# Optimization experiments

Hardware: AMD Instinct MI355X
Metric: run time of the kernel (lower is better)

The kernel has to match this reference:

```python
import jax, jax.numpy as jnp
import numpy as np

D = 128            # actual_dim / embed_dim
DM = 2 * D         # d_model
HID = 2 * DM       # LSTMCell hidden size
NSYM = 200000
PAD = NSYM
B = 4096
S = 5
NB = 64
STEPS = 4
EPS = 1e-6


def setup_inputs() -> dict:
    key = jax.random.key(0)
    ks = jax.random.split(key, 24)
    def rn(k, sh, scale=0.02):
        return jax.random.normal(k, sh, dtype=jnp.float32) * scale
    emb = rn(ks[10], (NSYM + 1, D)).at[PAD].set(0.0)  # padding row zeroed
    inp = {
        'query': jax.random.randint(ks[0], (B, 2), 0, NSYM),
        'support': jax.random.randint(ks[1], (S, 2), 0, NSYM),
        'q_l_conn': jax.random.randint(ks[2], (B, NB, 2), 0, NSYM),
        'q_l_deg': jax.random.randint(ks[3], (B,), 0, NB),
        'q_r_conn': jax.random.randint(ks[4], (B, NB, 2), 0, NSYM),
        'q_r_deg': jax.random.randint(ks[5], (B,), 0, NB),
        's_l_conn': jax.random.randint(ks[6], (S, NB, 2), 0, NSYM),
        's_l_deg': jax.random.randint(ks[7], (S,), 0, NB),
        's_r_conn': jax.random.randint(ks[8], (S, NB, 2), 0, NSYM),
        's_r_deg': jax.random.randint(ks[9], (S,), 0, NB),
        'emb': emb,
        'gcn_w': rn(ks[11], (D, 2 * D)),
        'gcn_bias': jnp.zeros((D,), jnp.float32),
        'proj1_w': rn(ks[12], (2 * DM, DM)),
        'proj1_b': jnp.zeros((2 * DM,), jnp.float32),
        'proj2_w': rn(ks[13], (DM, 2 * DM)),
        'proj2_b': jnp.zeros((DM,), jnp.float32),
        'ln_g': jnp.ones((DM,), jnp.float32),
        'ln_b': jnp.zeros((DM,), jnp.float32),
        'w_ih': rn(ks[14], (4 * HID, DM)),
        'w_hh': rn(ks[15], (4 * HID, HID)),
        'b_ih': jnp.zeros((4 * HID,), jnp.float32),
        'b_hh': jnp.zeros((4 * HID,), jnp.float32),
    }
    return inp


def _neighbor_encoder(conn, deg, emb, gcn_w, gcn_bias):
    # conn: [N, NB, 2] ids (rel, ent); deg: [N]
    rel = emb[conn[:, :, 0]]                     # [N, NB, D] gather
    ent = emb[conn[:, :, 1]]                     # [N, NB, D] gather
    x = jnp.concatenate([rel, ent], axis=-1)     # [N, NB, 2D]
    out = jnp.einsum('bnd,kd->bnk', x, gcn_w) + gcn_bias  # [N, NB, D]
    denom = jnp.maximum(deg, 1).astype(out.dtype)[:, None]
    return jnp.tanh(out.sum(axis=1) / denom)     # [N, D]


def _support_encoder(x, proj1_w, proj1_b, proj2_w, proj2_b, ln_g, ln_b):
    residual = x
    h = jax.nn.relu(x @ proj1_w.T + proj1_b)
    h = h @ proj2_w.T + proj2_b
    z = h + residual
    mu = z.mean(axis=-1, keepdims=True)
    sigma = jnp.std(z, axis=-1, keepdims=True, ddof=1)
    return ln_g * (z - mu) / (sigma + EPS) + ln_b


def _query_encoder(support_vec, query, w_ih, w_hh, b_ih, b_hh):
    # support_vec: [DM] (single support prototype); query: [B, DM]
    bsz = query.shape[0]
    h_r = jnp.zeros((bsz, HID), query.dtype)
    c = jnp.zeros((bsz, HID), query.dtype)
    xW = query @ w_ih.T + b_ih  # invariant across steps
    h = query
    for _ in range(STEPS):
        gates = xW + h_r @ w_hh.T + b_hh
        i, f, g, o = jnp.split(gates, 4, axis=-1)
        c = jax.nn.sigmoid(f) * c + jax.nn.sigmoid(i) * jnp.tanh(g)
        h_cell = jax.nn.sigmoid(o) * jnp.tanh(c)
        h = query + h_cell[:, :DM]
        # attention over a single support row: softmax of one logit == 1
        r = jnp.broadcast_to(support_vec[None, :], h.shape)
        h_r = jnp.concatenate([h, r], axis=-1)
    return h


def reference(query, support, q_l_conn, q_l_deg, q_r_conn, q_r_deg,
              s_l_conn, s_l_deg, s_r_conn, s_r_deg,
              emb, gcn_w, gcn_bias, proj1_w, proj1_b, proj2_w, proj2_b,
              ln_g, ln_b, w_ih, w_hh, b_ih, b_hh):
    ql = _neighbor_encoder(q_l_conn, q_l_deg, emb, gcn_w, gcn_bias)
    qr = _neighbor_encoder(q_r_conn, q_r_deg, emb, gcn_w, gcn_bias)
    sl = _neighbor_encoder(s_l_conn, s_l_deg, emb, gcn_w, gcn_bias)
    sr = _neighbor_encoder(s_r_conn, s_r_deg, emb, gcn_w, gcn_bias)
    query_nb = jnp.concatenate([ql, qr], axis=-1)    # [B, DM]
    support_nb = jnp.concatenate([sl, sr], axis=-1)  # [S, DM]
    se = lambda x: _support_encoder(x, proj1_w, proj1_b, proj2_w, proj2_b, ln_g, ln_b)
    support_g = se(support_nb).mean(axis=0)          # [DM]
    query_g = se(query_nb)                            # [B, DM]
    query_f = _query_encoder(support_g, query_g, w_ih, w_hh, b_ih, b_hh)
    qn = query_f / jnp.maximum(jnp.linalg.norm(query_f, axis=-1, keepdims=True), 1e-12)
    sn = support_g / jnp.maximum(jnp.linalg.norm(support_g), 1e-12)
    return qn @ sn                                    # [B] matching scores
```

## Files before the change

### kernel.cpp

```cpp
#include <hip/hip_runtime.h>

#define BQ 4096
#define NS 5

typedef __attribute__((ext_vector_type(8))) short bf16x8;
typedef __attribute__((ext_vector_type(4))) float f32x4;
typedef unsigned short ushortT;

#define WS_QNB    0
#define WS_Z      1048576
#define WS_QG     2097152
#define WS_XW     3145728
#define WS_CBUF   5242880
#define WS_XS     6291456
#define WS_H1B    7348224
#define WS_ABF    7872512
#define WS_HB1    8134656
#define WS_P1B    8396800
#define WS_P2B    8462336
#define WS_WIHB   8527872
#define WS_WHHB   8658944
#define WS_GWB    8790016
#define WS_SNB    8806400
#define WS_H1G    8807680
#define WS_ZB     8810240
#define WS_SG     8811520
#define WS_SN     8811776
#define WS_SWL    8812032
#define WS_BL     8813056

__device__ __forceinline__ float wave_allreduce(float v) {
#pragma unroll
  for (int off = 32; off > 0; off >>= 1) v += __shfl_xor(v, off, 64);
  return v;
}
__device__ __forceinline__ float block_allreduce(float v, float* buf) {
  v = wave_allreduce(v);
  __syncthreads();
  if ((threadIdx.x & 63) == 0) buf[threadIdx.x >> 6] = v;
  __syncthreads();
  return buf[0] + buf[1] + buf[2] + buf[3];
}
__device__ __forceinline__ float sigm(float x) { return 1.0f / (1.0f + expf(-x)); }
__device__ __forceinline__ ushortT f2bf(float f) {
  unsigned int u = __float_as_uint(f);
  unsigned int r = (u + 0x7fffu + ((u >> 16) & 1u)) >> 16;
  return (ushortT)r;
}
__device__ __forceinline__ float bf2f(ushortT u) {
  return __uint_as_float(((unsigned int)u) << 16);
}
__device__ __forceinline__ float dot4(float4 a, float4 b) {
  return a.x * b.x + a.y * b.y + a.z * b.z + a.w * b.w;
}

__global__ void k_pack(const float* __restrict__ w_ih, const float* __restrict__ w_hh,
                       const float* __restrict__ p1w, const float* __restrict__ p2w,
                       const float* __restrict__ gcn_w,
                       const float* __restrict__ b_ih, const float* __restrict__ b_hh,
                       ushortT* __restrict__ p1b16, ushortT* __restrict__ p2b16,
                       ushortT* __restrict__ wihb, ushortT* __restrict__ whhb,
                       ushortT* __restrict__ gwb, float* __restrict__ bL) {
  const int stride = gridDim.x * blockDim.x;
  const int gid = blockIdx.x * blockDim.x + threadIdx.x;
  for (int i = gid; i < 131072; i += stride) p1b16[i] = f2bf(p1w[i]);
  for (int i = gid; i < 131072; i += stride) p2b16[i] = f2bf(p2w[i]);
  for (int i = gid; i < 262144; i += stride) {
    int n = i >> 8, k = i & 255;
    int j = (n >> 2) + 512 * (n & 3);
    wihb[i] = f2bf(w_ih[j * 256 + k]);
    whhb[i] = f2bf(w_hh[j * 512 + k]);
  }
  for (int i = gid; i < 32768; i += stride) gwb[i] = f2bf(gcn_w[i]);
  for (int i = gid; i < 1024; i += stride) {
    int j = (i >> 2) + 512 * (i & 3);
    bL[i] = b_ih[j] + b_hh[j];
  }
}

__global__ __launch_bounds__(256) void k_gather(
    const int* __restrict__ qlc, const int* __restrict__ qrc,
    const int* __restrict__ slc, const int* __restrict__ src_,
    const float* __restrict__ emb, ushortT* __restrict__ XS) {
  const int r = blockIdx.x;
  const int b = r >> 1, side = r & 1;
  const int t = threadIdx.x;
  const int* cg;
  if (b < BQ) cg = (side ? qrc : qlc) + (size_t)b * 128;
  else        cg = (side ? src_ : slc) + (size_t)(b - BQ) * 128;
  __shared__ int connS[128];
  __shared__ __align__(16) float part[8][132];
  if (t < 128) connS[t] = cg[t];
  __syncthreads();
  const int s = t >> 5, l = t & 31;
  const float4* emb4 = (const float4*)emb;
  float4 acc = make_float4(0.f, 0.f, 0.f, 0.f);
#pragma unroll
  for (int kb = 0; kb < 2; kb++) {
    int im[8];
#pragma unroll
    for (int k = 0; k < 8; k++) im[k] = connS[(kb * 8 + k) * 8 + s];
    float4 v[8];
#pragma unroll
    for (int k = 0; k < 8; k++) v[k] = emb4[(size_t)im[k] * 32 + l];
#pragma unroll
    for (int k = 0; k < 8; k++) {
      acc.x += v[k].x; acc.y += v[k].y; acc.z += v[k].z; acc.w += v[k].w;
    }
  }
  *(float4*)&part[s][l * 4] = acc;
  __syncthreads();
  const int hf = t >> 7, dd = t & 127;
  float sum = part[hf][dd] + part[2 + hf][dd] + part[4 + hf][dd] + part[6 + hf][dd];
  XS[(size_t)r * 256 + t] = f2bf(sum);
}

__global__ __launch_bounds__(256) void k_gcn(
    const ushortT* __restrict__ XS, const ushortT* __restrict__ gwb,
    const float* __restrict__ gcn_bias,
    const int* __restrict__ qld, const int* __restrict__ qrd,
    const int* __restrict__ sld, const int* __restrict__ srd,
    float* __restrict__ qnb, float* __restrict__ snb, ushortT* __restrict__ xq) {
  __shared__ short As[64 * 40];
  __shared__ short Bs[128 * 40];
  __shared__ int degl[32], degr[32];
  const int t = threadIdx.x;
  const int row0 = blockIdx.x * 64;
  if (t < 32) {
    int b = (row0 >> 1) + t;
    int dl = 1, dr = 1;
    if (b < BQ) { dl = qld[b]; dr = qrd[b]; }
    else if (b < BQ + NS) { dl = sld[b - BQ]; dr = srd[b - BQ]; }
    degl[t] = (dl > 0) ? dl : 1;
    degr[t] = (dr > 0) ? dr : 1;
  }
  const int wave = t >> 6, lane = t & 63;
  const int wm = wave >> 1, wn = wave & 1, quad = lane >> 4, mr = lane & 15;
  f32x4 acc[2][4];
#pragma unroll
  for (int mi = 0; mi < 2; mi++)
#pragma unroll
    for (int ni = 0; ni < 4; ni++) acc[mi][ni] = (f32x4){0.f, 0.f, 0.f, 0.f};
  const int arow = t >> 2, akc = t & 3;
  for (int k0 = 0; k0 < 256; k0 += 32) {
    float4 av = *(const float4*)(XS + (size_t)(row0 + arow) * 256 + k0 + akc * 8);
    float4 bv0 = *(const float4*)(gwb + (size_t)arow * 256 + k0 + akc * 8);
    float4 bv1 = *(const float4*)(gwb + (size_t)(64 + arow) * 256 + k0 + akc * 8);
    __syncthreads();
    *(float4*)&As[arow * 40 + akc * 8] = av;
    *(float4*)&Bs[arow * 40 + akc * 8] = bv0;
    *(float4*)&Bs[(64 + arow) * 40 + akc * 8] = bv1;
    __syncthreads();
    bf16x8 af[2], bfr[4];
#pragma unroll
    for (int mi = 0; mi < 2; mi++)
      af[mi] = *(const bf16x8*)&As[(wm * 32 + mi * 16 + mr) * 40 + quad * 8];
#pragma unroll
    for (int ni = 0; ni < 4; ni++)
      bfr[ni] = *(const bf16x8*)&Bs[(wn * 64 + ni * 16 + mr) * 40 + quad * 8];
#pragma unroll
    for (int mi = 0; mi < 2; mi++)
#pragma unroll
      for (int ni = 0; ni < 4; ni++)
        acc[mi][ni] = __builtin_amdgcn_mfma_f32_16x16x32_bf16(af[mi], bfr[ni], acc[mi][ni], 0, 0, 0);
  }
#pragma unroll
  for (int mi = 0; mi < 2; mi++) {
#pragma unroll
    for (int ni = 0; ni < 4; ni++) {
      const int col = wn * 64 + ni * 16 + mr;
      const int rb = row0 + wm * 32 + mi * 16 + quad * 4;
      const float bs = 64.0f * gcn_bias[col];
#pragma unroll
      for (int reg = 0; reg < 4; reg++) {
        const int row = rb + reg;
        const int b = row >> 1, side = row & 1;
        if (b >= BQ + NS) continue;
        const int li = (row >> 1) - (row0 >> 1);
        const int deg = side ? degr[li] : degl[li];
        float val = tanhf((acc[mi][ni][reg] + bs) / (float)deg);
        if (b < BQ) {
          const size_t o = (size_t)b * 256 + side * 128 + col;
          qnb[o] = val;
          xq[o] = f2bf(val);
        } else {
          snb[(size_t)(b - BQ) * 256 + side * 128 + col] = val;
        }
      }
    }
  }
}

__global__ __launch_bounds__(256) void k_sup1(
    const float* __restrict__ snb, const float* __restrict__ p1w,
    const float* __restrict__ p1b, float* __restrict__ h1g) {
  const int w = blockIdx.x * 4 + (threadIdx.x >> 6);
  const int lane = threadIdx.x & 63;
  const int r = w >> 9, j = w & 511;
  float4 x = *(const float4*)&snb[r * 256 + lane * 4];
  float4 wv = *(const float4*)&p1w[(size_t)j * 256 + lane * 4];
  float s = wave_allreduce(dot4(x, wv));
  if (lane == 0) h1g[r * 512 + j] = fmaxf(s + p1b[j], 0.f);
}

__global__ __launch_bounds__(256) void k_sup2(
    const float* __restrict__ snb, const float* __restrict__ h1g,
    const float* __restrict__ p2w, const float* __restrict__ p2b,
    float* __restrict__ zb) {
  const int w = blockIdx.x * 4 + (threadIdx.x >> 6);
  const int lane = threadIdx.x & 63;
  const int r = w >> 8, tt = w & 255;
  float4 h0 = *(const float4*)&h1g[r * 512 + lane * 4];
  float4 h1 = *(const float4*)&h1g[r * 512 + 256 + lane * 4];
  float4 w0 = *(const float4*)&p2w[(size_t)tt * 512 + lane * 4];
  float4 w1 = *(const float4*)&p2w[(size_t)tt * 512 + 256 + lane * 4];
  float s = wave_allreduce(dot4(h0, w0) + dot4(h1, w1));
  if (lane == 0) zb[r * 256 + tt] = s + p2b[tt] + snb[r * 256 + tt];
}

__global__ __launch_bounds__(256) void k_sup3(
    const float* __restrict__ zb, const float* __restrict__ ln_g,
    const float* __restrict__ ln_b, float* __restrict__ sg, float* __restrict__ sn) {
  const int t = threadIdx.x;
  __shared__ float rbuf[4];
  float acc = 0.f;
  for (int r = 0; r < NS; r++) {
    float z = zb[r * 256 + t];
    float s = block_allreduce(z, rbuf);
    float mu = s * (1.f / 256.f);
    float dz = z - mu;
    float s2 = block_allreduce(dz * dz, rbuf);
    float rstd = 1.f / (sqrtf(s2 * (1.f / 255.f)) + 1e-6f);
    acc += ln_g[t] * dz * rstd + ln_b[t];
    __syncthreads();
  }
  float g = acc * (1.f / (float)NS);
  sg[t] = g;
  float n2 = block_allreduce(g * g, rbuf);
  sn[t] = g / fmaxf(sqrtf(n2), 1e-12f);
}

__global__ __launch_bounds__(256) void k_sup4(
    const float* __restrict__ sg, const float* __restrict__ w_hh,
    float* __restrict__ sWl) {
  const int n = blockIdx.x * 4 + (threadIdx.x >> 6);
  const int lane = threadIdx.x & 63;
  const int j = (n >> 2) + 512 * (n & 3);
  float4 x = *(const float4*)&sg[lane * 4];
  float4 wv = *(const float4*)&w_hh[(size_t)j * 512 + 256 + lane * 4];
  float s = wave_allreduce(dot4(x, wv));
  if (lane == 0) sWl[n] = s;
}

__global__ __launch_bounds__(256) void k_gemm(
    const ushortT* __restrict__ A, const ushortT* __restrict__ B,
    const float* __restrict__ bias, const float* __restrict__ aux,
    float* __restrict__ outf, ushortT* __restrict__ outb,
    int K, int N, int nbn, int mode) {
  __shared__ short As[64 * 40];
  __shared__ short Bs[128 * 40];
  const int t = threadIdx.x;
  const int bn = blockIdx.x % nbn, bm = blockIdx.x / nbn;
  const int row0 = bm * 64, col0 = bn * 128;
  const int wave = t >> 6, lane = t & 63;
  const int wm = wave >> 1, wn = wave & 1, quad = lane >> 4, mr = lane & 15;
  f32x4 acc[2][4];
#pragma unroll
  for (int mi = 0; mi < 2; mi++)
#pragma unroll
    for (int ni = 0; ni < 4; ni++) acc[mi][ni] = (f32x4){0.f, 0.f, 0.f, 0.f};
  const int arow = t >> 2, akc = t & 3;
  for (int k0 = 0; k0 < K; k0 += 32) {
    float4 av = *(const float4*)(A + (size_t)(row0 + arow) * K + k0 + akc * 8);
    float4 bv0 = *(const float4*)(B + (size_t)(col0 + arow) * K + k0 + akc * 8);
    float4 bv1 = *(const float4*)(B + (size_t)(col0 + 64 + arow) * K + k0 + akc * 8);
    __syncthreads();
    *(float4*)&As[arow * 40 + akc * 8] = av;
    *(float4*)&Bs[arow * 40 + akc * 8] = bv0;
    *(float4*)&Bs[(64 + arow) * 40 + akc * 8] = bv1;
    __syncthreads();
    bf16x8 af[2], bfr[4];
#pragma unroll
    for (int mi = 0; mi < 2; mi++)
      af[mi] = *(const bf16x8*)&As[(wm * 32 + mi * 16 + mr) * 40 + quad * 8];
#pragma unroll
    for (int ni = 0; ni < 4; ni++)
      bfr[ni] = *(const bf16x8*)&Bs[(wn * 64 + ni * 16 + mr) * 40 + quad * 8];
#pragma unroll
    for (int mi = 0; mi < 2; mi++)
#pragma unroll
      for (int ni = 0; ni < 4; ni++)
        acc[mi][ni] = __builtin_amdgcn_mfma_f32_16x16x32_bf16(af[mi], bfr[ni], acc[mi][ni], 0, 0, 0);
  }
#pragma unroll
  for (int mi = 0; mi < 2; mi++) {
#pragma unroll
    for (int ni = 0; ni < 4; ni++) {
      const int col = col0 + wn * 64 + ni * 16 + mr;
      const int rb = row0 + wm * 32 + mi * 16 + quad * 4;
      const float bs = bias[col];
#pragma unroll
      for (int reg = 0; reg < 4; reg++) {
        const int row = rb + reg;
        const size_t off = (size_t)row * N + col;
        float v = acc[mi][ni][reg];
        if (mode == 0) outb[off] = f2bf(fmaxf(v + bs, 0.f));
        else outf[off] = v + bs + aux[off];
      }
    }
  }
}

__global__ __launch_bounds__(256) void k_gemm_lstm(
    const ushortT* __restrict__ A, const ushortT* __restrict__ B,
    const float* __restrict__ bL, const float* __restrict__ sWl,
    const float* __restrict__ qg, ushortT* __restrict__ xwb,
    float* __restrict__ cbuf, ushortT* __restrict__ hb_out, int phase) {
  __shared__ short As[64 * 40];
  __shared__ short Bs[128 * 40];
  __shared__ __align__(16) float Cs[64 * 132];
  const int t = threadIdx.x;
  const int bn = blockIdx.x & 7, bm = blockIdx.x >> 3;
  const int row0 = bm * 64, col0 = bn * 128;
  const int wave = t >> 6, lane = t & 63;
  const int wm = wave >> 1, wn = wave & 1, quad = lane >> 4, mr = lane & 15;
  f32x4 acc[2][4];
#pragma unroll
  for (int mi = 0; mi < 2; mi++)
#pragma unroll
    for (int ni = 0; ni < 4; ni++) acc[mi][ni] = (f32x4){0.f, 0.f, 0.f, 0.f};
  const int arow = t >> 2, akc = t & 3;
  for (int k0 = 0; k0 < 256; k0 += 32) {
    float4 av = *(const float4*)(A + (size_t)(row0 + arow) * 256 + k0 + akc * 8);
    float4 bv0 = *(const float4*)(B + (size_t)(col0 + arow) * 256 + k0 + akc * 8);
    float4 bv1 = *(const float4*)(B + (size_t)(col0 + 64 + arow) * 256 + k0 + akc * 8);
    __syncthreads();
    *(float4*)&As[arow * 40 + akc * 8] = av;
    *(float4*)&Bs[arow * 40 + akc * 8] = bv0;
    *(float4*)&Bs[(64 + arow) * 40 + akc * 8] = bv1;
    __syncthreads();
    bf16x8 af[2], bfr[4];
#pragma unroll
    for (int mi = 0; mi < 2; mi++)
      af[mi] = *(const bf16x8*)&As[(wm * 32 + mi * 16 + mr) * 40 + quad * 8];
#pragma unroll
    for (int ni = 0; ni < 4; ni++)
      bfr[ni] = *(const bf16x8*)&Bs[(wn * 64 + ni * 16 + mr) * 40 + quad * 8];
#pragma unroll
    for (int mi = 0; mi < 2; mi++)
#pragma unroll
      for (int ni = 0; ni < 4; ni++)
        acc[mi][ni] = __builtin_amdgcn_mfma_f32_16x16x32_bf16(af[mi], bfr[ni], acc[mi][ni], 0, 0, 0);
  }
#pragma unroll
  for (int mi = 0; mi < 2; mi++)
#pragma unroll
    for (int ni = 0; ni < 4; ni++)
#pragma unroll
      for (int reg = 0; reg < 4; reg++)
        Cs[(wm * 32 + mi * 16 + quad * 4 + reg) * 132 + wn * 64 + ni * 16 + mr] =
            acc[mi][ni][reg];
  __syncthreads();
  const int u = t & 31, grp = t >> 5;
  const int ugl = bn * 32 + u;
#pragma unroll
  for (int i = 0; i < 8; i++) {
    const int rl = grp * 8 + i;
    const int row = row0 + rl;
    const size_t o = (size_t)row * 256 + ugl;
    float4 gv = *(const float4*)&Cs[rl * 132 + u * 4];
    if (phase == 0) {
      float4 bb = *(const float4*)&bL[col0 + u * 4];
      gv.x += bb.x; gv.y += bb.y; gv.z += bb.z; gv.w += bb.w;
      float c0 = sigm(gv.x) * tanhf(gv.z);
      float h = qg[o] + sigm(gv.w) * tanhf(c0);
      cbuf[o] = c0;
      hb_out[o] = f2bf(h);
      float4 sv = *(const float4*)&sWl[col0 + u * 4];
      ushort4 xo;
      xo.x = f2bf(gv.x + sv.x); xo.y = f2bf(gv.y + sv.y);
      xo.z = f2bf(gv.z + sv.z); xo.w = f2bf(gv.w + sv.w);
      *(ushort4*)&xwb[(size_t)row * 1024 + col0 + u * 4] = xo;
    } else {
      ushort4 xv = *(const ushort4*)&xwb[(size_t)row * 1024 + col0 + u * 4];
      gv.x += bf2f(xv.x); gv.y += bf2f(xv.y);
      gv.z += bf2f(xv.z); gv.w += bf2f(xv.w);
      float c = sigm(gv.y) * cbuf[o] + sigm(gv.x) * tanhf(gv.z);
      float h = qg[o] + sigm(gv.w) * tanhf(c);
      if (phase == 2) {
        cbuf[o] = h;
      } else {
        cbuf[o] = c;
        hb_out[o] = f2bf(h);
      }
    }
  }
}

__global__ __launch_bounds__(256) void k_ln(
    const float* __restrict__ Z, const float* __restrict__ ln_g,
    const float* __restrict__ ln_b, float* __restrict__ qg, ushortT* __restrict__ qgb) {
  const int t = threadIdx.x;
  const int row = blockIdx.x * 4 + (t >> 6);
  const int lane = t & 63;
  float4 z = *(const float4*)&Z[(size_t)row * 256 + lane * 4];
  float s = wave_allreduce(z.x + z.y + z.z + z.w);
  float mu = s * (1.f / 256.f);
  float dx = z.x - mu, dy = z.y - mu, dz = z.z - mu, dw = z.w - mu;
  float s2 = wave_allreduce(dx * dx + dy * dy + dz * dz + dw * dw);
  float rstd = 1.f / (sqrtf(s2 * (1.f / 255.f)) + 1e-6f);
  float4 g = *(const float4*)&ln_g[lane * 4];
  float4 bb = *(const float4*)&ln_b[lane * 4];
  float4 o;
  o.x = g.x * dx * rstd + bb.x;
  o.y = g.y * dy * rstd + bb.y;
  o.z = g.z * dz * rstd + bb.z;
  o.w = g.w * dw * rstd + bb.w;
  *(float4*)&qg[(size_t)row * 256 + lane * 4] = o;
  ushort4 u;
  u.x = f2bf(o.x); u.y = f2bf(o.y); u.z = f2bf(o.z); u.w = f2bf(o.w);
  *(ushort4*)&qgb[(size_t)row * 256 + lane * 4] = u;
}

__global__ __launch_bounds__(256) void k_out(
    const float* __restrict__ hf, const float* __restrict__ sn, float* __restrict__ out) {
  const int t = threadIdx.x;
  const int row = blockIdx.x * 4 + (t >> 6);
  const int lane = t & 63;
  float4 h = *(const float4*)&hf[(size_t)row * 256 + lane * 4];
  float4 s = *(const float4*)&sn[lane * 4];
  float dt = wave_allreduce(dot4(h, s));
  float nr = wave_allreduce(dot4(h, h));
  if (lane == 0) out[row] = dt / fmaxf(sqrtf(nr), 1e-12f);
}

extern "C" void kernel_launch(void* const* d_in, const int* in_sizes, int n_in,
                              void* d_out, int out_size, void* d_ws, size_t ws_size,
                              hipStream_t stream) {
  const int* q_l_conn = (const int*)d_in[2];
  const int* q_l_deg  = (const int*)d_in[3];
  const int* q_r_conn = (const int*)d_in[4];
  const int* q_r_deg  = (const int*)d_in[5];
  const int* s_l_conn = (const int*)d_in[6];
  const int* s_l_deg  = (const int*)d_in[7];
  const int* s_r_conn = (const int*)d_in[8];
  const int* s_r_deg  = (const int*)d_in[9];
  const float* emb      = (const float*)d_in[10];
  const float* gcn_w    = (const float*)d_in[11];
  const float* gcn_bias = (const float*)d_in[12];
  const float* proj1_w  = (const float*)d_in[13];
  const float* proj1_b  = (const float*)d_in[14];
  const float* proj2_w  = (const float*)d_in[15];
  const float* proj2_b  = (const float*)d_in[16];
  const float* ln_g     = (const float*)d_in[17];
  const float* ln_b     = (const float*)d_in[18];
  const float* w_ih     = (const float*)d_in[19];
  const float* w_hh     = (const float*)d_in[20];
  const float* b_ih     = (const float*)d_in[21];
  const float* b_hh     = (const float*)d_in[22];

  float* ws = (float*)d_ws;
  float* qnb   = ws + WS_QNB;
  float* Z     = ws + WS_Z;
  float* qg    = ws + WS_QG;
  ushortT* xwb = (ushortT*)(ws + WS_XW);
  float* cbuf  = ws + WS_CBUF;
  ushortT* XS    = (ushortT*)(ws + WS_XS);
  ushortT* h1b   = (ushortT*)(ws + WS_H1B);
  ushortT* abf   = (ushortT*)(ws + WS_ABF);
  ushortT* hb1   = (ushortT*)(ws + WS_HB1);
  ushortT* p1b16 = (ushortT*)(ws + WS_P1B);
  ushortT* p2b16 = (ushortT*)(ws + WS_P2B);
  ushortT* wihb  = (ushortT*)(ws + WS_WIHB);
  ushortT* whhb  = (ushortT*)(ws + WS_WHHB);
  ushortT* gwb   = (ushortT*)(ws + WS_GWB);
  float* snb   = ws + WS_SNB;
  float* h1g   = ws + WS_H1G;
  float* zb    = ws + WS_ZB;
  float* sg    = ws + WS_SG;
  float* sn    = ws + WS_SN;
  float* sWl   = ws + WS_SWL;
  float* bL    = ws + WS_BL;
  float* out   = (float*)d_out;

  hipLaunchKernelGGL(k_pack, dim3(512), dim3(256), 0, stream,
                     w_ih, w_hh, proj1_w, proj2_w, gcn_w, b_ih, b_hh,
                     p1b16, p2b16, wihb, whhb, gwb, bL);
  hipLaunchKernelGGL(k_gather, dim3(2 * (BQ + NS)), dim3(256), 0, stream,
                     q_l_conn, q_r_conn, s_l_conn, s_r_conn, emb, XS);
  hipLaunchKernelGGL(k_gcn, dim3(129), dim3(256), 0, stream,
                     XS, gwb, gcn_bias, q_l_deg, q_r_deg, s_l_deg, s_r_deg,
                     qnb, snb, abf);
  hipLaunchKernelGGL(k_sup1, dim3(640), dim3(256), 0, stream, snb, proj1_w, proj1_b, h1g);
  hipLaunchKernelGGL(k_sup2, dim3(320), dim3(256), 0, stream, snb, h1g, proj2_w, proj2_b, zb);
  hipLaunchKernelGGL(k_sup3, dim3(1), dim3(256), 0, stream, zb, ln_g, ln_b, sg, sn);
  hipLaunchKernelGGL(k_sup4, dim3(256), dim3(256), 0, stream, sg, w_hh, sWl);
  hipLaunchKernelGGL(k_gemm, dim3(64 * 4), dim3(256), 0, stream,
                     abf, p1b16, proj1_b, (const float*)nullptr, (float*)nullptr, h1b,
                     256, 512, 4, 0);
  hipLaunchKernelGGL(k_gemm, dim3(64 * 2), dim3(256), 0, stream,
                     h1b, p2b16, proj2_b, qnb, Z, (ushortT*)nullptr,
                     512, 256, 2, 1);
  hipLaunchKernelGGL(k_ln, dim3(BQ / 4), dim3(256), 0, stream, Z, ln_g, ln_b, qg, abf);
  hipLaunchKernelGGL(k_gemm_lstm, dim3(512), dim3(256), 0, stream,
                     abf, wihb, bL, sWl, qg, xwb, cbuf, hb1, 0);
  hipLaunchKernelGGL(k_gemm_lstm, dim3(512), dim3(256), 0, stream,
                     hb1, whhb, bL, sWl, qg, xwb, cbuf, abf, 1);
  hipLaunchKernelGGL(k_gemm_lstm, dim3(512), dim3(256), 0, stream,
                     abf, whhb, bL, sWl, qg, xwb, cbuf, hb1, 1);
  hipLaunchKernelGGL(k_gemm_lstm, dim3(512), dim3(256), 0, stream,
                     hb1, whhb, bL, sWl, qg, xwb, cbuf, (ushortT*)nullptr, 2);
  hipLaunchKernelGGL(k_out, dim3(BQ / 4), dim3(256), 0, stream, cbuf, sn, out);
}
```

Baseline: 359.8 us.

## Fuse projection, LayerNorm, LSTM steps and scoring into one kernel; gather bf16 embeddings

Replaces the two projection GEMMs, the LayerNorm kernel, the four LSTM GEMM kernels and the output kernel with one kernel. Each block owns 16 query rows and keeps the activations, gate pre-activations, cell state and hidden state in LDS and registers, with weights streamed from global memory. This removes several launches and the global round-trips of the Z, qg, xw, cbuf and h buffers. Separately, the embedding table is converted to bf16 on every call so the random gather reads half as many bytes. The cost is one full pass over the table each call, plus lower occupancy and repeated L2 weight reads in the fused kernel.

Result: slower. 369.8 us (+2.8%).

```diff
diff --git a/kernel.cpp b/kernel.cpp
--- a/kernel.cpp
+++ b/kernel.cpp
@@ -7,27 +7,37 @@
 typedef __attribute__((ext_vector_type(4))) float f32x4;
 typedef unsigned short ushortT;
 
-#define WS_QNB    0
-#define WS_Z      1048576
-#define WS_QG     2097152
-#define WS_XW     3145728
-#define WS_CBUF   5242880
-#define WS_XS     6291456
-#define WS_H1B    7348224
-#define WS_ABF    7872512
-#define WS_HB1    8134656
-#define WS_P1B    8396800
-#define WS_P2B    8462336
-#define WS_WIHB   8527872
-#define WS_WHHB   8658944
-#define WS_GWB    8790016
-#define WS_SNB    8806400
-#define WS_H1G    8807680
-#define WS_ZB     8810240
-#define WS_SG     8811520
-#define WS_SN     8811776
-#define WS_SWL    8812032
-#define WS_BL     8813056
+constexpr size_t BF(size_t nshorts) { return (nshorts + 1) / 2; }
+constexpr size_t RUP(size_t x, size_t m) { return (x + m - 1) / m * m; }
+constexpr size_t NR_XS = RUP(2 * (BQ + NS), 64);
+constexpr size_t WS_EMBB = 0;
+constexpr size_t SZ_EMBB = BF((size_t)200001 * 128);
+constexpr size_t WS_QNB  = 0;
+constexpr size_t SZ_QNB  = (size_t)BQ * 256;
+constexpr size_t WS_XS   = WS_EMBB + SZ_EMBB;
+constexpr size_t SZ_XS   = BF(NR_XS * 256);
+constexpr size_t WS_ABF  = WS_XS + SZ_XS;
+constexpr size_t SZ_ABF  = BF((size_t)BQ * 256);
+constexpr size_t WS_P1B  = WS_ABF + SZ_ABF;
+constexpr size_t SZ_P1B  = BF((size_t)512 * 256);
+constexpr size_t WS_P2B  = WS_P1B + SZ_P1B;
+constexpr size_t SZ_P2B  = BF((size_t)256 * 512);
+constexpr size_t WS_WIHB = WS_P2B + SZ_P2B;
+constexpr size_t SZ_WIHB = BF((size_t)1024 * 256);
+constexpr size_t WS_WHHB = WS_WIHB + SZ_WIHB;
+constexpr size_t SZ_WHHB = BF((size_t)1024 * 256);
+constexpr size_t WS_GWB  = WS_WHHB + SZ_WHHB;
+constexpr size_t SZ_GWB  = BF((size_t)128 * 256);
+constexpr size_t WS_SNB  = WS_GWB + SZ_GWB;
+constexpr size_t WS_H1G  = WS_SNB + NS * 256;
+constexpr size_t WS_ZB   = WS_H1G + NS * 512;
+constexpr size_t WS_SG   = WS_ZB + NS * 256;
+constexpr size_t WS_SN   = WS_SG + 256;
+constexpr size_t WS_SWL  = WS_SN + 256;
+constexpr size_t WS_BL   = WS_SWL + 1024;
+constexpr size_t WS_TOTAL = WS_BL + 1024;
+static_assert(WS_ABF - WS_XS == 1056768, "XS size (8256 rows x 256 bf16)");
+static_assert(WS_P1B - WS_ABF == 524288, "ABF size (4096x256 bf16)");
 
 __device__ __forceinline__ float wave_allreduce(float v) {
 #pragma unroll
@@ -52,6 +62,19 @@
 }
 __device__ __forceinline__ float dot4(float4 a, float4 b) {
   return a.x * b.x + a.y * b.y + a.z * b.z + a.w * b.w;
+}
+
+__global__ __launch_bounds__(256) void k_ebf(const float* __restrict__ emb,
+                                             ushortT* __restrict__ embb) {
+  const int stride = gridDim.x * blockDim.x;
+  const float4* e4 = (const float4*)emb;
+  ushort4* o4 = (ushort4*)embb;
+  for (int i = blockIdx.x * blockDim.x + threadIdx.x; i < 6400032; i += stride) {
+    float4 v = e4[i];
+    ushort4 u;
+    u.x = f2bf(v.x); u.y = f2bf(v.y); u.z = f2bf(v.z); u.w = f2bf(v.w);
+    o4[i] = u;
+  }
 }
 
 __global__ void k_pack(const float* __restrict__ w_ih, const float* __restrict__ w_hh,
@@ -81,7 +104,7 @@
 __global__ __launch_bounds__(256) void k_gather(
     const int* __restrict__ qlc, const int* __restrict__ qrc,
     const int* __restrict__ slc, const int* __restrict__ src_,
-    const float* __restrict__ emb, ushortT* __restrict__ XS) {
+    const ushortT* __restrict__ embb, ushortT* __restrict__ XS) {
   const int r = blockIdx.x;
   const int b = r >> 1, side = r & 1;
   const int t = threadIdx.x;
@@ -93,19 +116,20 @@
   if (t < 128) connS[t] = cg[t];
   __syncthreads();
   const int s = t >> 5, l = t & 31;
-  const float4* emb4 = (const float4*)emb;
   float4 acc = make_float4(0.f, 0.f, 0.f, 0.f);
 #pragma unroll
   for (int kb = 0; kb < 2; kb++) {
     int im[8];
 #pragma unroll
     for (int k = 0; k < 8; k++) im[k] = connS[(kb * 8 + k) * 8 + s];
-    float4 v[8];
-#pragma unroll
-    for (int k = 0; k < 8; k++) v[k] = emb4[(size_t)im[k] * 32 + l];
+    ushort4 v[8];
+#pragma unroll
+    for (int k = 0; k < 8; k++)
+      v[k] = ((const ushort4*)(embb + (size_t)im[k] * 128))[l];
 #pragma unroll
     for (int k = 0; k < 8; k++) {
-      acc.x += v[k].x; acc.y += v[k].y; acc.z += v[k].z; acc.w += v[k].w;
+      acc.x += bf2f(v[k].x); acc.y += bf2f(v[k].y);
+      acc.z += bf2f(v[k].z); acc.w += bf2f(v[k].w);
     }
   }
   *(float4*)&part[s][l * 4] = acc;
@@ -252,186 +276,203 @@
   if (lane == 0) sWl[n] = s;
 }
 
-__global__ __launch_bounds__(256) void k_gemm(
-    const ushortT* __restrict__ A, const ushortT* __restrict__ B,
-    const float* __restrict__ bias, const float* __restrict__ aux,
-    float* __restrict__ outf, ushortT* __restrict__ outb,
-    int K, int N, int nbn, int mode) {
-  __shared__ short As[64 * 40];
-  __shared__ short Bs[128 * 40];
+template <int KCH>
+__device__ __forceinline__ void gemm_pass(
+    const ushortT* __restrict__ Alds, int astride,
+    const ushortT* __restrict__ Bg, int bstride, int colbase,
+    float (*Cs)[260], int wave, int lane) {
+  const int quad = lane >> 4, mr = lane & 15;
+  f32x4 acc[4];
+#pragma unroll
+  for (int ni = 0; ni < 4; ni++) acc[ni] = (f32x4){0.f, 0.f, 0.f, 0.f};
+  const ushortT* arow = Alds + mr * astride + quad * 8;
+#pragma unroll
+  for (int k0 = 0; k0 < KCH; k0++) {
+    bf16x8 af = *(const bf16x8*)(arow + k0 * 32);
+#pragma unroll
+    for (int ni = 0; ni < 4; ni++) {
+      const ushortT* bp = Bg + (size_t)(colbase + wave * 64 + ni * 16 + mr) * bstride
+                          + k0 * 32 + quad * 8;
+      bf16x8 bf = *(const bf16x8*)bp;
+      acc[ni] = __builtin_amdgcn_mfma_f32_16x16x32_bf16(af, bf, acc[ni], 0, 0, 0);
+    }
+  }
+#pragma unroll
+  for (int ni = 0; ni < 4; ni++)
+#pragma unroll
+    for (int reg = 0; reg < 4; reg++)
+      Cs[quad * 4 + reg][wave * 64 + ni * 16 + mr] = acc[ni][reg];
+}
+
+__global__ __launch_bounds__(256) void k_fused(
+    const ushortT* __restrict__ xq, const float* __restrict__ qnb,
+    const ushortT* __restrict__ p1b16, const float* __restrict__ p1bias,
+    const ushortT* __restrict__ p2b16, const float* __restrict__ p2bias,
+    const float* __restrict__ ln_g, const float* __restrict__ ln_b,
+    const ushortT* __restrict__ wihb, const ushortT* __restrict__ whhb,
+    const float* __restrict__ bL, const float* __restrict__ sWl,
+    const float* __restrict__ sn, float* __restrict__ outv) {
+  __shared__ __align__(16) ushortT xwS[16 * 1024];
+  __shared__ __align__(16) ushortT hS[16 * 272];
+  __shared__ __align__(16) float Cs[16][260];
+  __shared__ float snS[256];
   const int t = threadIdx.x;
-  const int bn = blockIdx.x % nbn, bm = blockIdx.x / nbn;
-  const int row0 = bm * 64, col0 = bn * 128;
   const int wave = t >> 6, lane = t & 63;
-  const int wm = wave >> 1, wn = wave & 1, quad = lane >> 4, mr = lane & 15;
-  f32x4 acc[2][4];
-#pragma unroll
-  for (int mi = 0; mi < 2; mi++)
-#pragma unroll
-    for (int ni = 0; ni < 4; ni++) acc[mi][ni] = (f32x4){0.f, 0.f, 0.f, 0.f};
-  const int arow = t >> 2, akc = t & 3;
-  for (int k0 = 0; k0 < K; k0 += 32) {
-    float4 av = *(const float4*)(A + (size_t)(row0 + arow) * K + k0 + akc * 8);
-    float4 bv0 = *(const float4*)(B + (size_t)(col0 + arow) * K + k0 + akc * 8);
-    float4 bv1 = *(const float4*)(B + (size_t)(col0 + 64 + arow) * K + k0 + akc * 8);
-    __syncthreads();
-    *(float4*)&As[arow * 40 + akc * 8] = av;
-    *(float4*)&Bs[arow * 40 + akc * 8] = bv0;
-    *(float4*)&Bs[(64 + arow) * 40 + akc * 8] = bv1;
-    __syncthreads();
-    bf16x8 af[2], bfr[4];
-#pragma unroll
-    for (int mi = 0; mi < 2; mi++)
-      af[mi] = *(const bf16x8*)&As[(wm * 32 + mi * 16 + mr) * 40 + quad * 8];
-#pragma unroll
-    for (int ni = 0; ni < 4; ni++)
-      bfr[ni] = *(const bf16x8*)&Bs[(wn * 64 + ni * 16 + mr) * 40 + quad * 8];
-#pragma unroll
-    for (int mi = 0; mi < 2; mi++)
-#pragma unroll
-      for (int ni = 0; ni < 4; ni++)
-        acc[mi][ni] = __builtin_amdgcn_mfma_f32_16x16x32_bf16(af[mi], bfr[ni], acc[mi][ni], 0, 0, 0);
-  }
-#pragma unroll
-  for (int mi = 0; mi < 2; mi++) {
-#pragma unroll
-    for (int ni = 0; ni < 4; ni++) {
-      const int col = col0 + wn * 64 + ni * 16 + mr;
-      const int rb = row0 + wm * 32 + mi * 16 + quad * 4;
-      const float bs = bias[col];
-#pragma unroll
-      for (int reg = 0; reg < 4; reg++) {
-        const int row = rb + reg;
-        const size_t off = (size_t)row * N + col;
-        float v = acc[mi][ni][reg];
-        if (mode == 0) outb[off] = f2bf(fmaxf(v + bs, 0.f));
-        else outf[off] = v + bs + aux[off];
-      }
-    }
-  }
-}
-
-__global__ __launch_bounds__(256) void k_gemm_lstm(
-    const ushortT* __restrict__ A, const ushortT* __restrict__ B,
-    const float* __restrict__ bL, const float* __restrict__ sWl,
-    const float* __restrict__ qg, ushortT* __restrict__ xwb,
-    float* __restrict__ cbuf, ushortT* __restrict__ hb_out, int phase) {
-  __shared__ short As[64 * 40];
-  __shared__ short Bs[128 * 40];
-  __shared__ __align__(16) float Cs[64 * 132];
-  const int t = threadIdx.x;
-  const int bn = blockIdx.x & 7, bm = blockIdx.x >> 3;
-  const int row0 = bm * 64, col0 = bn * 128;
-  const int wave = t >> 6, lane = t & 63;
-  const int wm = wave >> 1, wn = wave & 1, quad = lane >> 4, mr = lane & 15;
-  f32x4 acc[2][4];
-#pragma unroll
-  for (int mi = 0; mi < 2; mi++)
-#pragma unroll
-    for (int ni = 0; ni < 4; ni++) acc[mi][ni] = (f32x4){0.f, 0.f, 0.f, 0.f};
-  const int arow = t >> 2, akc = t & 3;
-  for (int k0 = 0; k0 < 256; k0 += 32) {
-    float4 av = *(const float4*)(A + (size_t)(row0 + arow) * 256 + k0 + akc * 8);
-    float4 bv0 = *(const float4*)(B + (size_t)(col0 + arow) * 256 + k0 + akc * 8);
-    float4 bv1 = *(const float4*)(B + (size_t)(col0 + 64 + arow) * 256 + k0 + akc * 8);
-    __syncthreads();
-    *(float4*)&As[arow * 40 + akc * 8] = av;
-    *(float4*)&Bs[arow * 40 + akc * 8] = bv0;
-    *(float4*)&Bs[(64 + arow) * 40 + akc * 8] = bv1;
-    __syncthreads();
-    bf16x8 af[2], bfr[4];
-#pragma unroll
-    for (int mi = 0; mi < 2; mi++)
-      af[mi] = *(const bf16x8*)&As[(wm * 32 + mi * 16 + mr) * 40 + quad * 8];
-#pragma unroll
-    for (int ni = 0; ni < 4; ni++)
-      bfr[ni] = *(const bf16x8*)&Bs[(wn * 64 + ni * 16 + mr) * 40 + quad * 8];
-#pragma unroll
-    for (int mi = 0; mi < 2; mi++)
-#pragma unroll
-      for (int ni = 0; ni < 4; ni++)
-        acc[mi][ni] = __builtin_amdgcn_mfma_f32_16x16x32_bf16(af[mi], bfr[ni], acc[mi][ni], 0, 0, 0);
-  }
-#pragma unroll
-  for (int mi = 0; mi < 2; mi++)
-#pragma unroll
-    for (int ni = 0; ni < 4; ni++)
-#pragma unroll
-      for (int reg = 0; reg < 4; reg++)
-        Cs[(wm * 32 + mi * 16 + quad * 4 + reg) * 132 + wn * 64 + ni * 16 + mr] =
-            acc[mi][ni][reg];
-  __syncthreads();
-  const int u = t & 31, grp = t >> 5;
-  const int ugl = bn * 32 + u;
-#pragma unroll
-  for (int i = 0; i < 8; i++) {
-    const int rl = grp * 8 + i;
-    const int row = row0 + rl;
-    const size_t o = (size_t)row * 256 + ugl;
-    float4 gv = *(const float4*)&Cs[rl * 132 + u * 4];
-    if (phase == 0) {
-      float4 bb = *(const float4*)&bL[col0 + u * 4];
+  const int row0 = blockIdx.x * 16;
+  ushortT* h1S = xwS;
+
+  {
+    const int r = t >> 4, c = (t & 15) * 16;
+    const float4* src = (const float4*)(xq + (size_t)(row0 + r) * 256 + c);
+    *(float4*)&hS[r * 272 + c] = src[0];
+    *(float4*)&hS[r * 272 + c + 8] = src[1];
+    snS[t] = sn[t];
+  }
+  __syncthreads();
+
+#pragma unroll
+  for (int p = 0; p < 2; p++) {
+    gemm_pass<8>(hS, 272, p1b16, 256, p * 256, Cs, wave, lane);
+    __syncthreads();
+    const int c4 = (t & 63) * 4;
+#pragma unroll
+    for (int i = 0; i < 4; i++) {
+      const int row = (t >> 6) + 4 * i;
+      float4 v = *(const float4*)&Cs[row][c4];
+      float4 bb = *(const float4*)&p1bias[p * 256 + c4];
+      ushort4 o;
+      o.x = f2bf(fmaxf(v.x + bb.x, 0.f));
+      o.y = f2bf(fmaxf(v.y + bb.y, 0.f));
+      o.z = f2bf(fmaxf(v.z + bb.z, 0.f));
+      o.w = f2bf(fmaxf(v.w + bb.w, 0.f));
+      *(ushort4*)&h1S[row * 520 + p * 256 + c4] = o;
+    }
+    __syncthreads();
+  }
+
+  gemm_pass<16>(h1S, 520, p2b16, 512, 0, Cs, wave, lane);
+  __syncthreads();
+  {
+    const int row = t >> 4, li = t & 15;
+    float4 zr[4];
+    float sum = 0.f;
+#pragma unroll
+    for (int j = 0; j < 4; j++) {
+      const int c = li * 16 + j * 4;
+      float4 v = *(const float4*)&Cs[row][c];
+      float4 bb = *(const float4*)&p2bias[c];
+      float4 xv = *(const float4*)&qnb[(size_t)(row0 + row) * 256 + c];
+      v.x += bb.x + xv.x; v.y += bb.y + xv.y;
+      v.z += bb.z + xv.z; v.w += bb.w + xv.w;
+      zr[j] = v;
+      sum += v.x + v.y + v.z + v.w;
+    }
+#pragma unroll
+    for (int m = 1; m < 16; m <<= 1) sum += __shfl_xor(sum, m, 64);
+    const float mu = sum * (1.f / 256.f);
+    float s2 = 0.f;
+#pragma unroll
+    for (int j = 0; j < 4; j++) {
+      float dx = zr[j].x - mu, dy = zr[j].y - mu, dz = zr[j].z - mu, dw = zr[j].w - mu;
+      s2 += dx * dx + dy * dy + dz * dz + dw * dw;
+    }
+#pragma unroll
+    for (int m = 1; m < 16; m <<= 1) s2 += __shfl_xor(s2, m, 64);
+    const float rstd = 1.f / (sqrtf(s2 * (1.f / 255.f)) + 1e-6f);
+#pragma unroll
+    for (int j = 0; j < 4; j++) {
+      const int c = li * 16 + j * 4;
+      float4 g = *(const float4*)&ln_g[c];
+      float4 b = *(const float4*)&ln_b[c];
+      float4 q;
+      q.x = g.x * (zr[j].x - mu) * rstd + b.x;
+      q.y = g.y * (zr[j].y - mu) * rstd + b.y;
+      q.z = g.z * (zr[j].z - mu) * rstd + b.z;
+      q.w = g.w * (zr[j].w - mu) * rstd + b.w;
+      *(float4*)&Cs[row][c] = q;
+      ushort4 o;
+      o.x = f2bf(q.x); o.y = f2bf(q.y); o.z = f2bf(q.z); o.w = f2bf(q.w);
+      *(ushort4*)&hS[row * 272 + c] = o;
+    }
+  }
+  __syncthreads();
+
+  const int l6 = t & 63;
+  float q_reg[4][4], c_reg[4][4], h_reg[4][4];
+#pragma unroll
+  for (int i = 0; i < 4; i++)
+#pragma unroll
+    for (int p = 0; p < 4; p++)
+      q_reg[i][p] = Cs[(t >> 6) + 4 * i][p * 64 + l6];
+  __syncthreads();
+
+#pragma unroll
+  for (int p = 0; p < 4; p++) {
+    gemm_pass<8>(hS, 272, wihb, 256, p * 256, Cs, wave, lane);
+    __syncthreads();
+    float4 sv = *(const float4*)&sWl[p * 256 + l6 * 4];
+    float4 bb = *(const float4*)&bL[p * 256 + l6 * 4];
+#pragma unroll
+    for (int i = 0; i < 4; i++) {
+      const int row = (t >> 6) + 4 * i;
+      float4 gv = *(const float4*)&Cs[row][l6 * 4];
       gv.x += bb.x; gv.y += bb.y; gv.z += bb.z; gv.w += bb.w;
       float c0 = sigm(gv.x) * tanhf(gv.z);
-      float h = qg[o] + sigm(gv.w) * tanhf(c0);
-      cbuf[o] = c0;
-      hb_out[o] = f2bf(h);
-      float4 sv = *(const float4*)&sWl[col0 + u * 4];
+      float h = q_reg[i][p] + sigm(gv.w) * tanhf(c0);
+      c_reg[i][p] = c0;
+      h_reg[i][p] = h;
       ushort4 xo;
       xo.x = f2bf(gv.x + sv.x); xo.y = f2bf(gv.y + sv.y);
       xo.z = f2bf(gv.z + sv.z); xo.w = f2bf(gv.w + sv.w);
-      *(ushort4*)&xwb[(size_t)row * 1024 + col0 + u * 4] = xo;
-    } else {
-      ushort4 xv = *(const ushort4*)&xwb[(size_t)row * 1024 + col0 + u * 4];
-      gv.x += bf2f(xv.x); gv.y += bf2f(xv.y);
-      gv.z += bf2f(xv.z); gv.w += bf2f(xv.w);
-      float c = sigm(gv.y) * cbuf[o] + sigm(gv.x) * tanhf(gv.z);
-      float h = qg[o] + sigm(gv.w) * tanhf(c);
-      if (phase == 2) {
-        cbuf[o] = h;
-      } else {
-        cbuf[o] = c;
-        hb_out[o] = f2bf(h);
+      *(ushort4*)&xwS[row * 1024 + p * 256 + l6 * 4] = xo;
+      if (p == 3) {
+#pragma unroll
+        for (int pp = 0; pp < 4; pp++)
+          hS[row * 272 + pp * 64 + l6] = f2bf(h_reg[i][pp]);
       }
     }
-  }
-}
-
-__global__ __launch_bounds__(256) void k_ln(
-    const float* __restrict__ Z, const float* __restrict__ ln_g,
-    const float* __restrict__ ln_b, float* __restrict__ qg, ushortT* __restrict__ qgb) {
-  const int t = threadIdx.x;
-  const int row = blockIdx.x * 4 + (t >> 6);
-  const int lane = t & 63;
-  float4 z = *(const float4*)&Z[(size_t)row * 256 + lane * 4];
-  float s = wave_allreduce(z.x + z.y + z.z + z.w);
-  float mu = s * (1.f / 256.f);
-  float dx = z.x - mu, dy = z.y - mu, dz = z.z - mu, dw = z.w - mu;
-  float s2 = wave_allreduce(dx * dx + dy * dy + dz * dz + dw * dw);
-  float rstd = 1.f / (sqrtf(s2 * (1.f / 255.f)) + 1e-6f);
-  float4 g = *(const float4*)&ln_g[lane * 4];
-  float4 bb = *(const float4*)&ln_b[lane * 4];
-  float4 o;
-  o.x = g.x * dx * rstd + bb.x;
-  o.y = g.y * dy * rstd + bb.y;
-  o.z = g.z * dz * rstd + bb.z;
-  o.w = g.w * dw * rstd + bb.w;
-  *(float4*)&qg[(size_t)row * 256 + lane * 4] = o;
-  ushort4 u;
-  u.x = f2bf(o.x); u.y = f2bf(o.y); u.z = f2bf(o.z); u.w = f2bf(o.w);
-  *(ushort4*)&qgb[(size_t)row * 256 + lane * 4] = u;
-}
-
-__global__ __launch_bounds__(256) void k_out(
-    const float* __restrict__ hf, const float* __restrict__ sn, float* __restrict__ out) {
-  const int t = threadIdx.x;
-  const int row = blockIdx.x * 4 + (t >> 6);
-  const int lane = t & 63;
-  float4 h = *(const float4*)&hf[(size_t)row * 256 + lane * 4];
-  float4 s = *(const float4*)&sn[lane * 4];
-  float dt = wave_allreduce(dot4(h, s));
-  float nr = wave_allreduce(dot4(h, h));
-  if (lane == 0) out[row] = dt / fmaxf(sqrtf(nr), 1e-12f);
+    __syncthreads();
+  }
+
+  float dotv[4] = {0.f, 0.f, 0.f, 0.f}, nrmv[4] = {0.f, 0.f, 0.f, 0.f};
+  for (int s = 1; s < 4; s++) {
+    const int last = (s == 3);
+#pragma unroll
+    for (int p = 0; p < 4; p++) {
+      gemm_pass<8>(hS, 272, whhb, 256, p * 256, Cs, wave, lane);
+      __syncthreads();
+#pragma unroll
+      for (int i = 0; i < 4; i++) {
+        const int row = (t >> 6) + 4 * i;
+        float4 gv = *(const float4*)&Cs[row][l6 * 4];
+        ushort4 xv = *(const ushort4*)&xwS[row * 1024 + p * 256 + l6 * 4];
+        gv.x += bf2f(xv.x); gv.y += bf2f(xv.y);
+        gv.z += bf2f(xv.z); gv.w += bf2f(xv.w);
+        float c = sigm(gv.y) * c_reg[i][p] + sigm(gv.x) * tanhf(gv.z);
+        float h = q_reg[i][p] + sigm(gv.w) * tanhf(c);
+        c_reg[i][p] = c;
+        if (last) {
+          dotv[i] += h * snS[p * 64 + l6];
+          nrmv[i] += h * h;
+        } else {
+          h_reg[i][p] = h;
+          if (p == 3) {
+#pragma unroll
+            for (int pp = 0; pp < 4; pp++)
+              hS[row * 272 + pp * 64 + l6] = f2bf(h_reg[i][pp]);
+          }
+        }
+      }
+      __syncthreads();
+    }
+  }
+
+#pragma unroll
+  for (int i = 0; i < 4; i++) {
+    float d = wave_allreduce(dotv[i]);
+    float n = wave_allreduce(nrmv[i]);
+    if (lane == 0) outv[row0 + wave + 4 * i] = d / fmaxf(sqrtf(n), 1e-12f);
+  }
 }
 
 extern "C" void kernel_launch(void* const* d_in, const int* in_sizes, int n_in,
@@ -460,15 +501,10 @@
   const float* b_hh     = (const float*)d_in[22];
 
   float* ws = (float*)d_ws;
-  float* qnb   = ws + WS_QNB;
-  float* Z     = ws + WS_Z;
-  float* qg    = ws + WS_QG;
-  ushortT* xwb = (ushortT*)(ws + WS_XW);
-  float* cbuf  = ws + WS_CBUF;
+  ushortT* embb  = (ushortT*)(ws + WS_EMBB);
+  float* qnb     = ws + WS_QNB;
   ushortT* XS    = (ushortT*)(ws + WS_XS);
-  ushortT* h1b   = (ushortT*)(ws + WS_H1B);
   ushortT* abf   = (ushortT*)(ws + WS_ABF);
-  ushortT* hb1   = (ushortT*)(ws + WS_HB1);
   ushortT* p1b16 = (ushortT*)(ws + WS_P1B);
   ushortT* p2b16 = (ushortT*)(ws + WS_P2B);
   ushortT* wihb  = (ushortT*)(ws + WS_WIHB);
@@ -483,11 +519,12 @@
   float* bL    = ws + WS_BL;
   float* out   = (float*)d_out;
 
+  hipLaunchKernelGGL(k_ebf, dim3(2048), dim3(256), 0, stream, emb, embb);
   hipLaunchKernelGGL(k_pack, dim3(512), dim3(256), 0, stream,
                      w_ih, w_hh, proj1_w, proj2_w, gcn_w, b_ih, b_hh,
                      p1b16, p2b16, wihb, whhb, gwb, bL);
   hipLaunchKernelGGL(k_gather, dim3(2 * (BQ + NS)), dim3(256), 0, stream,
-                     q_l_conn, q_r_conn, s_l_conn, s_r_conn, emb, XS);
+                     q_l_conn, q_r_conn, s_l_conn, s_r_conn, embb, XS);
   hipLaunchKernelGGL(k_gcn, dim3(129), dim3(256), 0, stream,
                      XS, gwb, gcn_bias, q_l_deg, q_r_deg, s_l_deg, s_r_deg,
                      qnb, snb, abf);
@@ -495,20 +532,7 @@
   hipLaunchKernelGGL(k_sup2, dim3(320), dim3(256), 0, stream, snb, h1g, proj2_w, proj2_b, zb);
   hipLaunchKernelGGL(k_sup3, dim3(1), dim3(256), 0, stream, zb, ln_g, ln_b, sg, sn);
   hipLaunchKernelGGL(k_sup4, dim3(256), dim3(256), 0, stream, sg, w_hh, sWl);
-  hipLaunchKernelGGL(k_gemm, dim3(64 * 4), dim3(256), 0, stream,
-                     abf, p1b16, proj1_b, (const float*)nullptr, (float*)nullptr, h1b,
-                     256, 512, 4, 0);
-  hipLaunchKernelGGL(k_gemm, dim3(64 * 2), dim3(256), 0, stream,
-                     h1b, p2b16, proj2_b, qnb, Z, (ushortT*)nullptr,
-                     512, 256, 2, 1);
-  hipLaunchKernelGGL(k_ln, dim3(BQ / 4), dim3(256), 0, stream, Z, ln_g, ln_b, qg, abf);
-  hipLaunchKernelGGL(k_gemm_lstm, dim3(512), dim3(256), 0, stream,
-                     abf, wihb, bL, sWl, qg, xwb, cbuf, hb1, 0);
-  hipLaunchKernelGGL(k_gemm_lstm, dim3(512), dim3(256), 0, stream,
-                     hb1, whhb, bL, sWl, qg, xwb, cbuf, abf, 1);
-  hipLaunchKernelGGL(k_gemm_lstm, dim3(512), dim3(256), 0, stream,
-                     abf, whhb, bL, sWl, qg, xwb, cbuf, hb1, 1);
-  hipLaunchKernelGGL(k_gemm_lstm, dim3(512), dim3(256), 0, stream,
-                     hb1, whhb, bL, sWl, qg, xwb, cbuf, (ushortT*)nullptr, 2);
-  hipLaunchKernelGGL(k_out, dim3(BQ / 4), dim3(256), 0, stream, cbuf, sn, out);
-}
+  hipLaunchKernelGGL(k_fused, dim3(BQ / 16), dim3(256), 0, stream,
+                     abf, qnb, p1b16, proj1_b, p2b16, proj2_b, ln_g, ln_b,
+                     wihb, whhb, bL, sWl, sn, out);
+}
```
